# Optimization experiments

Hardware: AMD Instinct MI355X
Metric: run time of the kernel (lower is better)

The kernel has to match this reference:

```python
import jax, jax.numpy as jnp
import numpy as np

B, C, H, W = 16, 512, 14, 14
OUT = 8192
EPS_SQRT = 1e-5
EPS_NORM = 1e-12


def _make_sketch(key, input_dim, output_dim):
    kh, ks = jax.random.split(key)
    rand_h = jax.random.randint(kh, (input_dim,), 0, output_dim)
    rand_s = (2 * jax.random.randint(ks, (input_dim,), 0, 2) - 1).astype(jnp.float32)
    # count-sketch matrix densified: one nonzero (+-1) per row
    S = jnp.zeros((input_dim, output_dim), dtype=jnp.float32)
    return S.at[jnp.arange(input_dim), rand_h].set(rand_s)


def setup_inputs() -> dict:
    key = jax.random.key(0)
    kx, k1, k2 = jax.random.split(key, 3)
    x = jax.random.normal(kx, (B, C, H, W), dtype=jnp.float32)
    sketch1 = _make_sketch(k1, C, OUT)
    sketch2 = _make_sketch(k2, C, OUT)
    return {"x": x, "sketch1": sketch1, "sketch2": sketch2}


def reference(x, sketch1, sketch2):
    output_dim = sketch1.shape[1]
    # [B,C,H,W] -> [B,H,W,C] then project with count-sketch matrices -> [B,H,W,OUT]
    xp = jnp.transpose(x, (0, 2, 3, 1))
    p1 = xp @ sketch1
    p2 = xp @ sketch2
    # circular convolution via FFT (torch.rfft unnormalized; torch.irfft has 1/n, then *output_dim)
    f1 = jnp.fft.rfft(p1, axis=-1)
    f2 = jnp.fft.rfft(p2, axis=-1)
    cbp = jnp.fft.irfft(f1 * f2, n=output_dim, axis=-1) * output_dim
    # sum-pool over spatial dims -> [B, OUT]
    X = cbp.sum(axis=(1, 2))
    # signed square-root
    X = jnp.sign(X) * jnp.sqrt(jnp.abs(X) + EPS_SQRT)
    # L2 normalize per row (F.normalize semantics)
    norm = jnp.maximum(jnp.linalg.norm(X, axis=-1, keepdims=True), EPS_NORM)
    return X / norm
```

## Files before the change

### kernel.cpp

```cpp
#include <hip/hip_runtime.h>
#include <math.h>

#define OUT_DIM 8192
#define C_DIM   512
#define B_DIM   16
#define HW      196
#define LROW    40
#define PL      (128 * LROW)

typedef __attribute__((ext_vector_type(8))) short bf16x8;
typedef __attribute__((ext_vector_type(4))) float f32x4;

__global__ __launch_bounds__(256) void prep(
    const float* __restrict__ S1, const float* __restrict__ S2,
    int* __restrict__ h1, float* __restrict__ s1,
    int* __restrict__ h2, float* __restrict__ s2,
    float* __restrict__ ss)
{
    const int bid = blockIdx.x;
    const int t = threadIdx.x;
    int row = bid & 511;
    const float* S = (bid < 512) ? S1 : S2;
    int* h = (bid < 512) ? h1 : h2;
    float* s = (bid < 512) ? s1 : s2;
    const float4* p = (const float4*)(S + (size_t)row * OUT_DIM);
#pragma unroll
    for (int m = 0; m < 8; ++m) {
        int q = t + m * 256;
        float4 v = p[q];
        int base = q * 4;
        if (v.x != 0.f) { h[row] = base + 0; s[row] = v.x; }
        if (v.y != 0.f) { h[row] = base + 1; s[row] = v.y; }
        if (v.z != 0.f) { h[row] = base + 2; s[row] = v.z; }
        if (v.w != 0.f) { h[row] = base + 3; s[row] = v.w; }
    }
    if (bid == 0 && t < B_DIM) ss[t] = 0.f;
}

__global__ __launch_bounds__(512) void gram_mfma(
    const float* __restrict__ x,
    const int* __restrict__ h1, const float* __restrict__ s1,
    const int* __restrict__ h2, const float* __restrict__ s2,
    float* __restrict__ partials)
{
    __shared__ __align__(16) unsigned short lds[4 * PL];

    const int bid = blockIdx.x;
    const int xcd = bid & 7;
    const int idx = bid >> 3;
    const int b   = xcd + 8 * (idx & 1);
    const int tile = idx >> 1;
    const int c1b = (tile >> 2) * 128, c2b = (tile & 3) * 128;

    const int t = threadIdx.x;
    const int l = t & 63, w = t >> 6;
    const int wr = w >> 2, wc = w & 3;
    const int lrow = l & 15, lk = l >> 4;

    const float* xb = x + (size_t)b * C_DIM * HW;

    const int row0 = t >> 2, grp0 = t & 3;
    const float* srcA = xb + (size_t)(c1b + row0) * HW + grp0 * 8;
    const float* srcB = xb + (size_t)(c2b + row0) * HW + grp0 * 8;

    f32x4 acc[4][2];
#pragma unroll
    for (int m = 0; m < 4; ++m)
#pragma unroll
        for (int n = 0; n < 2; ++n) acc[m][n] = (f32x4){0.f, 0.f, 0.f, 0.f};

    float4 a0, a1, b0, b1;
    const float4 z4 = make_float4(0.f, 0.f, 0.f, 0.f);

    a0 = *(const float4*)(srcA);     a1 = *(const float4*)(srcA + 4);
    b0 = *(const float4*)(srcB);     b1 = *(const float4*)(srcB + 4);

#pragma unroll
    for (int kc = 0; kc < 7; ++kc) {
        __syncthreads();
        {
            float va[8] = {a0.x, a0.y, a0.z, a0.w, a1.x, a1.y, a1.z, a1.w};
            float vb[8] = {b0.x, b0.y, b0.z, b0.w, b1.x, b1.y, b1.z, b1.w};
            bf16x8 ahv, alv, bhv, blv;
#pragma unroll
            for (int e = 0; e < 8; ++e) {
                unsigned int ua = __float_as_uint(va[e]);
                float haf = __uint_as_float(ua & 0xFFFF0000u);
                ahv[e] = (short)(ua >> 16);
                alv[e] = (short)(__float_as_uint(va[e] - haf) >> 16);
                unsigned int ub = __float_as_uint(vb[e]);
                float hbf = __uint_as_float(ub & 0xFFFF0000u);
                bhv[e] = (short)(ub >> 16);
                blv[e] = (short)(__float_as_uint(vb[e] - hbf) >> 16);
            }
            unsigned short* dst = lds + row0 * LROW + grp0 * 8;
            *(bf16x8*)(dst + 0 * PL) = ahv;
            *(bf16x8*)(dst + 1 * PL) = alv;
            *(bf16x8*)(dst + 2 * PL) = bhv;
            *(bf16x8*)(dst + 3 * PL) = blv;
        }
        __syncthreads();
        if (kc < 6) {
            const int kn = (kc + 1) * 32;
            if (kc + 1 < 6) {
                a0 = *(const float4*)(srcA + kn); a1 = *(const float4*)(srcA + kn + 4);
                b0 = *(const float4*)(srcB + kn); b1 = *(const float4*)(srcB + kn + 4);
            } else {
                a1 = z4; b1 = z4;
                a0 = (grp0 == 0) ? *(const float4*)(srcA + 192) : z4;
                b0 = (grp0 == 0) ? *(const float4*)(srcB + 192) : z4;
            }
        }
        bf16x8 ah[4], al[4], bh[2], bl[2];
#pragma unroll
        for (int m = 0; m < 4; ++m) {
            int r = wr * 64 + m * 16 + lrow;
            ah[m] = *(const bf16x8*)(lds + 0 * PL + r * LROW + lk * 8);
            al[m] = *(const bf16x8*)(lds + 1 * PL + r * LROW + lk * 8);
        }
#pragma unroll
        for (int n = 0; n < 2; ++n) {
            int r = wc * 32 + n * 16 + lrow;
            bh[n] = *(const bf16x8*)(lds + 2 * PL + r * LROW + lk * 8);
            bl[n] = *(const bf16x8*)(lds + 3 * PL + r * LROW + lk * 8);
        }
#pragma unroll
        for (int m = 0; m < 4; ++m)
#pragma unroll
            for (int n = 0; n < 2; ++n) {
                acc[m][n] = __builtin_amdgcn_mfma_f32_16x16x32_bf16(ah[m], bh[n], acc[m][n], 0, 0, 0);
                acc[m][n] = __builtin_amdgcn_mfma_f32_16x16x32_bf16(ah[m], bl[n], acc[m][n], 0, 0, 0);
                acc[m][n] = __builtin_amdgcn_mfma_f32_16x16x32_bf16(al[m], bh[n], acc[m][n], 0, 0, 0);
            }
    }

    int   hh1[4][4]; float sv1[4][4];
    int   hh2[2];    float sv2[2];
#pragma unroll
    for (int m = 0; m < 4; ++m)
#pragma unroll
        for (int r = 0; r < 4; ++r) {
            int c1 = c1b + wr * 64 + m * 16 + lk * 4 + r;
            hh1[m][r] = h1[c1]; sv1[m][r] = s1[c1];
        }
#pragma unroll
    for (int n = 0; n < 2; ++n) {
        int c2 = c2b + wc * 32 + n * 16 + lrow;
        hh2[n] = h2[c2]; sv2[n] = s2[c2];
    }

    __syncthreads();
    float* bins = (float*)lds;
    for (int mm = t; mm < OUT_DIM; mm += 512) bins[mm] = 0.f;
    __syncthreads();
#pragma unroll
    for (int m = 0; m < 4; ++m)
#pragma unroll
        for (int n = 0; n < 2; ++n)
#pragma unroll
            for (int r = 0; r < 4; ++r) {
                int bin = (hh1[m][r] + hh2[n]) & (OUT_DIM - 1);
                atomicAdd(&bins[bin], acc[m][n][r] * sv1[m][r] * sv2[n]);
            }
    __syncthreads();

    float* outp = partials + (size_t)(b * 16 + tile) * OUT_DIM;
    for (int mm = t; mm < OUT_DIM; mm += 512) outp[mm] = bins[mm];
}

__global__ __launch_bounds__(256) void fin_a(
    float* __restrict__ partials, float* __restrict__ ss)
{
    const int b = blockIdx.x >> 4, ch = blockIdx.x & 15, t = threadIdx.x;
    float sq = 0.f;
    float vals[2];
    int ks[2];
#pragma unroll
    for (int i = 0; i < 2; ++i) {
        int k = ch * 512 + i * 256 + t;
        ks[i] = k;
        float a = 0.f;
#pragma unroll
        for (int tile = 0; tile < 16; ++tile)
            a += partials[(size_t)(b * 16 + tile) * OUT_DIM + k];
        a *= (float)OUT_DIM;
        float sg = (a > 0.f) ? 1.f : ((a < 0.f) ? -1.f : 0.f);
        vals[i] = sg * sqrtf(fabsf(a) + 1e-5f);
        sq += fabsf(a) + 1e-5f;
    }
#pragma unroll
    for (int off = 32; off; off >>= 1) sq += __shfl_down(sq, off, 64);
    __shared__ float red[4];
    if ((t & 63) == 0) red[t >> 6] = sq;
    __syncthreads();
    if (t == 0) atomicAdd(&ss[b], red[0] + red[1] + red[2] + red[3]);
#pragma unroll
    for (int i = 0; i < 2; ++i)
        partials[(size_t)(b * 16) * OUT_DIM + ks[i]] = vals[i];
}

__global__ __launch_bounds__(256) void fin_b(
    const float* __restrict__ partials, const float* __restrict__ ss,
    float* __restrict__ out)
{
    const int b = blockIdx.x >> 4, ch = blockIdx.x & 15, t = threadIdx.x;
    float inv = 1.f / fmaxf(sqrtf(ss[b]), 1e-12f);
#pragma unroll
    for (int i = 0; i < 2; ++i) {
        int k = ch * 512 + i * 256 + t;
        out[(size_t)b * OUT_DIM + k] = partials[(size_t)(b * 16) * OUT_DIM + k] * inv;
    }
}

extern "C" void kernel_launch(void* const* d_in, const int* in_sizes, int n_in,
                              void* d_out, int out_size, void* d_ws, size_t ws_size,
                              hipStream_t stream) {
    const float* x   = (const float*)d_in[0];
    const float* sk1 = (const float*)d_in[1];
    const float* sk2 = (const float*)d_in[2];

    char* ws = (char*)d_ws;
    int*   h1 = (int*)(ws);
    float* s1 = (float*)(ws + 2048);
    int*   h2 = (int*)(ws + 4096);
    float* s2 = (float*)(ws + 6144);
    float* ss = (float*)(ws + 8192);
    float* partials = (float*)(ws + 8448);

    prep<<<1024, 256, 0, stream>>>(sk1, sk2, h1, s1, h2, s2, ss);
    gram_mfma<<<256, 512, 0, stream>>>(x, h1, s1, h2, s2, partials);
    fin_a<<<256, 256, 0, stream>>>(partials, ss);
    fin_b<<<256, 256, 0, stream>>>(partials, ss, (float*)d_out);
}
```

Before: 121.3 us.

## Pre-split x into MFMA-fragment bf16 hi/lo layout in prep kernel

The prep kernel gains extra blocks that convert x into bf16 hi/lo planes stored directly in the per-lane MFMA fragment layout in global workspace. The gram kernel then loads fragments straight from global memory with register double-buffering instead of staging through LDS with barriers. It also drops to 256 threads with a larger 4x4 per-wave tile. The aim is to remove the LDS round-trip, the per-tile redundant conversions and the syncs. In exchange it adds a global write and read of the split planes and more register pressure.

```diff
diff --git a/kernel.cpp b/kernel.cpp
--- a/kernel.cpp
+++ b/kernel.cpp
@@ -5,45 +5,84 @@
 #define C_DIM   512
 #define B_DIM   16
 #define HW      196
-#define LROW    40
-#define PL      (128 * LROW)
 
 typedef __attribute__((ext_vector_type(8))) short bf16x8;
 typedef __attribute__((ext_vector_type(4))) float f32x4;
 
+
 __global__ __launch_bounds__(256) void prep(
+    const float* __restrict__ x,
     const float* __restrict__ S1, const float* __restrict__ S2,
     int* __restrict__ h1, float* __restrict__ s1,
     int* __restrict__ h2, float* __restrict__ s2,
+    unsigned short* __restrict__ PH, unsigned short* __restrict__ PLo,
     float* __restrict__ ss)
 {
     const int bid = blockIdx.x;
     const int t = threadIdx.x;
-    int row = bid & 511;
-    const float* S = (bid < 512) ? S1 : S2;
-    int* h = (bid < 512) ? h1 : h2;
-    float* s = (bid < 512) ? s1 : s2;
-    const float4* p = (const float4*)(S + (size_t)row * OUT_DIM);
-#pragma unroll
-    for (int m = 0; m < 8; ++m) {
-        int q = t + m * 256;
-        float4 v = p[q];
-        int base = q * 4;
-        if (v.x != 0.f) { h[row] = base + 0; s[row] = v.x; }
-        if (v.y != 0.f) { h[row] = base + 1; s[row] = v.y; }
-        if (v.z != 0.f) { h[row] = base + 2; s[row] = v.z; }
-        if (v.w != 0.f) { h[row] = base + 3; s[row] = v.w; }
-    }
-    if (bid == 0 && t < B_DIM) ss[t] = 0.f;
-}
-
-__global__ __launch_bounds__(512) void gram_mfma(
-    const float* __restrict__ x,
+
+    if (bid < 1024) {
+        int row = bid & 511;
+        const float* S = (bid < 512) ? S1 : S2;
+        int* h = (bid < 512) ? h1 : h2;
+        float* s = (bid < 512) ? s1 : s2;
+        const float4* p = (const float4*)(S + (size_t)row * OUT_DIM);
+#pragma unroll
+        for (int m = 0; m < 8; ++m) {
+            int q = t + m * 256;
+            float4 v = p[q];
+            int base = q * 4;
+            if (v.x != 0.f) { h[row] = base + 0; s[row] = v.x; }
+            if (v.y != 0.f) { h[row] = base + 1; s[row] = v.y; }
+            if (v.z != 0.f) { h[row] = base + 2; s[row] = v.z; }
+            if (v.w != 0.f) { h[row] = base + 3; s[row] = v.w; }
+        }
+        if (bid == 0 && t < B_DIM) ss[t] = 0.f;
+        return;
+    }
+
+    const int u = bid - 1024;
+    const int b = u >> 5, rb = u & 31;
+    __shared__ float xs[16 * HW];
+    const float* src = x + ((size_t)b * C_DIM + rb * 16) * HW;
+#pragma unroll
+    for (int i = 0; i < 13; ++i) {
+        int idx = t + i * 256;
+        if (idx < 16 * HW) xs[idx] = src[idx];
+    }
+    __syncthreads();
+
+    const int r = t & 15, u0 = t >> 4;
+#pragma unroll
+    for (int p = 0; p < 2; ++p) {
+        int unit = u0 + p * 16;
+        if (unit < 28) {
+            bf16x8 hv, lv;
+#pragma unroll
+            for (int e = 0; e < 8; ++e) {
+                int k = unit * 8 + e;
+                float v = (k < HW) ? xs[r * HW + k] : 0.f;
+                unsigned int uv = __float_as_uint(v);
+                unsigned short hi = (unsigned short)(uv >> 16);
+                float hif = __uint_as_float(((unsigned int)hi) << 16);
+                hv[e] = (short)hi;
+                lv[e] = (short)(__float_as_uint(v - hif) >> 16);
+            }
+            int kb = unit >> 2, lk = unit & 3;
+            size_t base = ((((size_t)b * 32 + rb) * 7 + kb) * 4 + lk) * 128 + r * 8;
+            *(bf16x8*)(PH + base) = hv;
+            *(bf16x8*)(PLo + base) = lv;
+        }
+    }
+}
+
+__global__ __launch_bounds__(256) void gram_mfma(
+    const unsigned short* __restrict__ PH, const unsigned short* __restrict__ PLo,
     const int* __restrict__ h1, const float* __restrict__ s1,
     const int* __restrict__ h2, const float* __restrict__ s2,
     float* __restrict__ partials)
 {
-    __shared__ __align__(16) unsigned short lds[4 * PL];
+    __shared__ float bins[OUT_DIM];
 
     const int bid = blockIdx.x;
     const int xcd = bid & 7;
@@ -54,88 +93,57 @@
 
     const int t = threadIdx.x;
     const int l = t & 63, w = t >> 6;
-    const int wr = w >> 2, wc = w & 3;
+    const int wr = w >> 1, wc = w & 1;
+
+    for (int mm = t; mm < OUT_DIM; mm += 256) bins[mm] = 0.f;
+
+    const size_t arb0 = ((size_t)b * 32 + (c1b >> 4) + wr * 4) * 7;
+    const size_t brb0 = ((size_t)b * 32 + (c2b >> 4) + wc * 4) * 7;
+    const int loff = l * 8;
+
+#define FRAG(P, rbase, m, kb) (*(const bf16x8*)((P) + ((rbase) + (size_t)(m) * 7 + (kb)) * 512 + loff))
+
+    f32x4 acc[4][4];
+#pragma unroll
+    for (int m = 0; m < 4; ++m)
+#pragma unroll
+        for (int n = 0; n < 4; ++n) acc[m][n] = (f32x4){0.f, 0.f, 0.f, 0.f};
+
+    bf16x8 ah[2][4], al[2][4], bh[2][4], bl[2][4];
+#pragma unroll
+    for (int m = 0; m < 4; ++m) {
+        ah[0][m] = FRAG(PH,  arb0, m, 0);
+        al[0][m] = FRAG(PLo, arb0, m, 0);
+        bh[0][m] = FRAG(PH,  brb0, m, 0);
+        bl[0][m] = FRAG(PLo, brb0, m, 0);
+    }
+
+#pragma unroll
+    for (int kb = 0; kb < 7; ++kb) {
+        const int cur = kb & 1, nxt = cur ^ 1;
+        if (kb < 6) {
+#pragma unroll
+            for (int m = 0; m < 4; ++m) {
+                ah[nxt][m] = FRAG(PH,  arb0, m, kb + 1);
+                al[nxt][m] = FRAG(PLo, arb0, m, kb + 1);
+                bh[nxt][m] = FRAG(PH,  brb0, m, kb + 1);
+                bl[nxt][m] = FRAG(PLo, brb0, m, kb + 1);
+            }
+        }
+#pragma unroll
+        for (int m = 0; m < 4; ++m)
+#pragma unroll
+            for (int n = 0; n < 4; ++n) {
+                acc[m][n] = __builtin_amdgcn_mfma_f32_16x16x32_bf16(ah[cur][m], bh[cur][n], acc[m][n], 0, 0, 0);
+                acc[m][n] = __builtin_amdgcn_mfma_f32_16x16x32_bf16(ah[cur][m], bl[cur][n], acc[m][n], 0, 0, 0);
+                acc[m][n] = __builtin_amdgcn_mfma_f32_16x16x32_bf16(al[cur][m], bh[cur][n], acc[m][n], 0, 0, 0);
+            }
+    }
+#undef FRAG
+
     const int lrow = l & 15, lk = l >> 4;
-
-    const float* xb = x + (size_t)b * C_DIM * HW;
-
-    const int row0 = t >> 2, grp0 = t & 3;
-    const float* srcA = xb + (size_t)(c1b + row0) * HW + grp0 * 8;
-    const float* srcB = xb + (size_t)(c2b + row0) * HW + grp0 * 8;
-
-    f32x4 acc[4][2];
-#pragma unroll
-    for (int m = 0; m < 4; ++m)
-#pragma unroll
-        for (int n = 0; n < 2; ++n) acc[m][n] = (f32x4){0.f, 0.f, 0.f, 0.f};
-
-    float4 a0, a1, b0, b1;
-    const float4 z4 = make_float4(0.f, 0.f, 0.f, 0.f);
-
-    a0 = *(const float4*)(srcA);     a1 = *(const float4*)(srcA + 4);
-    b0 = *(const float4*)(srcB);     b1 = *(const float4*)(srcB + 4);
-
-#pragma unroll
-    for (int kc = 0; kc < 7; ++kc) {
-        __syncthreads();
-        {
-            float va[8] = {a0.x, a0.y, a0.z, a0.w, a1.x, a1.y, a1.z, a1.w};
-            float vb[8] = {b0.x, b0.y, b0.z, b0.w, b1.x, b1.y, b1.z, b1.w};
-            bf16x8 ahv, alv, bhv, blv;
-#pragma unroll
-            for (int e = 0; e < 8; ++e) {
-                unsigned int ua = __float_as_uint(va[e]);
-                float haf = __uint_as_float(ua & 0xFFFF0000u);
-                ahv[e] = (short)(ua >> 16);
-                alv[e] = (short)(__float_as_uint(va[e] - haf) >> 16);
-                unsigned int ub = __float_as_uint(vb[e]);
-                float hbf = __uint_as_float(ub & 0xFFFF0000u);
-                bhv[e] = (short)(ub >> 16);
-                blv[e] = (short)(__float_as_uint(vb[e] - hbf) >> 16);
-            }
-            unsigned short* dst = lds + row0 * LROW + grp0 * 8;
-            *(bf16x8*)(dst + 0 * PL) = ahv;
-            *(bf16x8*)(dst + 1 * PL) = alv;
-            *(bf16x8*)(dst + 2 * PL) = bhv;
-            *(bf16x8*)(dst + 3 * PL) = blv;
-        }
-        __syncthreads();
-        if (kc < 6) {
-            const int kn = (kc + 1) * 32;
-            if (kc + 1 < 6) {
-                a0 = *(const float4*)(srcA + kn); a1 = *(const float4*)(srcA + kn + 4);
-                b0 = *(const float4*)(srcB + kn); b1 = *(const float4*)(srcB + kn + 4);
-            } else {
-                a1 = z4; b1 = z4;
-                a0 = (grp0 == 0) ? *(const float4*)(srcA + 192) : z4;
-                b0 = (grp0 == 0) ? *(const float4*)(srcB + 192) : z4;
-            }
-        }
-        bf16x8 ah[4], al[4], bh[2], bl[2];
-#pragma unroll
-        for (int m = 0; m < 4; ++m) {
-            int r = wr * 64 + m * 16 + lrow;
-            ah[m] = *(const bf16x8*)(lds + 0 * PL + r * LROW + lk * 8);
-            al[m] = *(const bf16x8*)(lds + 1 * PL + r * LROW + lk * 8);
-        }
-#pragma unroll
-        for (int n = 0; n < 2; ++n) {
-            int r = wc * 32 + n * 16 + lrow;
-            bh[n] = *(const bf16x8*)(lds + 2 * PL + r * LROW + lk * 8);
-            bl[n] = *(const bf16x8*)(lds + 3 * PL + r * LROW + lk * 8);
-        }
-#pragma unroll
-        for (int m = 0; m < 4; ++m)
-#pragma unroll
-            for (int n = 0; n < 2; ++n) {
-                acc[m][n] = __builtin_amdgcn_mfma_f32_16x16x32_bf16(ah[m], bh[n], acc[m][n], 0, 0, 0);
-                acc[m][n] = __builtin_amdgcn_mfma_f32_16x16x32_bf16(ah[m], bl[n], acc[m][n], 0, 0, 0);
-                acc[m][n] = __builtin_amdgcn_mfma_f32_16x16x32_bf16(al[m], bh[n], acc[m][n], 0, 0, 0);
-            }
-    }
-
     int   hh1[4][4]; float sv1[4][4];
-    int   hh2[2];    float sv2[2];
+    int   hh2[4];    float sv2[4];
 #pragma unroll
     for (int m = 0; m < 4; ++m)
 #pragma unroll
@@ -144,19 +152,16 @@
             hh1[m][r] = h1[c1]; sv1[m][r] = s1[c1];
         }
 #pragma unroll
-    for (int n = 0; n < 2; ++n) {
-        int c2 = c2b + wc * 32 + n * 16 + lrow;
+    for (int n = 0; n < 4; ++n) {
+        int c2 = c2b + wc * 64 + n * 16 + lrow;
         hh2[n] = h2[c2]; sv2[n] = s2[c2];
     }
 
     __syncthreads();
-    float* bins = (float*)lds;
-    for (int mm = t; mm < OUT_DIM; mm += 512) bins[mm] = 0.f;
-    __syncthreads();
 #pragma unroll
     for (int m = 0; m < 4; ++m)
 #pragma unroll
-        for (int n = 0; n < 2; ++n)
+        for (int n = 0; n < 4; ++n)
 #pragma unroll
             for (int r = 0; r < 4; ++r) {
                 int bin = (hh1[m][r] + hh2[n]) & (OUT_DIM - 1);
@@ -165,7 +170,7 @@
     __syncthreads();
 
     float* outp = partials + (size_t)(b * 16 + tile) * OUT_DIM;
-    for (int mm = t; mm < OUT_DIM; mm += 512) outp[mm] = bins[mm];
+    for (int mm = t; mm < OUT_DIM; mm += 256) outp[mm] = bins[mm];
 }
 
 __global__ __launch_bounds__(256) void fin_a(
@@ -226,9 +231,11 @@
     float* s2 = (float*)(ws + 6144);
     float* ss = (float*)(ws + 8192);
     float* partials = (float*)(ws + 8448);
-
-    prep<<<1024, 256, 0, stream>>>(sk1, sk2, h1, s1, h2, s2, ss);
-    gram_mfma<<<256, 512, 0, stream>>>(x, h1, s1, h2, s2, partials);
+    unsigned short* PH  = (unsigned short*)(ws + 8397056);
+    unsigned short* PLo = (unsigned short*)(ws + 15737088);
+
+    prep<<<1536, 256, 0, stream>>>(x, sk1, sk2, h1, s1, h2, s2, PH, PLo, ss);
+    gram_mfma<<<256, 256, 0, stream>>>(PH, PLo, h1, s1, h2, s2, partials);
     fin_a<<<256, 256, 0, stream>>>(partials, ss);
     fin_b<<<256, 256, 0, stream>>>(partials, ss, (float*)d_out);
 }
```

After: 121.1 us. About the same (-0.2%).
